# Performance work log

Hardware: AMD Instinct MI355X
Metric: run time of the kernel (lower is better)

The kernel has to match this reference:

```python
import jax, jax.numpy as jnp
import numpy as np


def conv2d(x, w, b=None):
    # NCHW conv, stride 1, 'same' padding inferred from kernel size
    ph, pw = w.shape[2] // 2, w.shape[3] // 2
    y = jax.lax.conv_general_dilated(
        x, w, window_strides=(1, 1), padding=[(ph, ph), (pw, pw)],
        dimension_numbers=('NCHW', 'OIHW', 'NCHW'))
    if b is not None:
        y = y + b[None, :, None, None]
    return y


def gelu(v):
    return jax.nn.gelu(v, approximate=False)  # torch nn.GELU default (erf)


def lrelu(v):
    return jnp.where(v >= 0, v, 0.1 * v)  # LeakyReLU(0.1)


def setup_inputs() -> dict:
    key = jax.random.key(0)
    ks = jax.random.split(key, 16)
    B, C, H, W = 2, 32, 256, 256
    s = 0.05
    return {
        'x':      jax.random.normal(ks[0], (B, C, H, W), jnp.float32),
        'key':    jax.random.normal(ks[1], (B, C, H, W), jnp.float32),
        'w_off1': jax.random.normal(ks[2], (32, 64, 3, 3), jnp.float32) * s,
        'b_off1': jax.random.normal(ks[3], (32,), jnp.float32) * s,
        'w_off2': jax.random.normal(ks[4], (32, 32, 3, 3), jnp.float32) * s,
        'b_off2': jax.random.normal(ks[5], (32,), jnp.float32) * s,
        'w_dcn':  jax.random.normal(ks[6], (288, 64, 3, 3), jnp.float32) * s,
        'b_dcn':  jax.random.normal(ks[7], (288,), jnp.float32) * s,
        'w_sel':  jax.random.normal(ks[8], (1, 3, 3, 3), jnp.float32) * s,
        'b_sel':  jax.random.normal(ks[9], (1,), jnp.float32) * s,
        'w_t1':   jax.random.normal(ks[10], (32, 32, 3, 3), jnp.float32) * s,
        'w_t2':   jax.random.normal(ks[11], (128, 32, 1, 1), jnp.float32) * s,
        'w_t3':   jax.random.normal(ks[12], (128, 128, 3, 3), jnp.float32) * s,
        'w_t4':   jax.random.normal(ks[13], (32, 128, 1, 1), jnp.float32) * s,
        'w_t5':   jax.random.normal(ks[14], (32, 32, 3, 3), jnp.float32) * s,
    }


def reference(x, key, w_off1, b_off1, w_off2, b_off2, w_dcn, b_dcn,
              w_sel, b_sel, w_t1, w_t2, w_t3, w_t4, w_t5):
    B, C, H, W = x.shape
    TOPK = 3
    # offset branch
    off = lrelu(conv2d(jnp.concatenate([x, key], axis=1), w_off1, b_off1))
    off = lrelu(conv2d(off, w_off2, b_off2))
    # dcn_attention proxy: conv over (key, offset) producing C*9 candidate warps
    warp = conv2d(jnp.concatenate([key, off], axis=1), w_dcn, b_dcn)
    warp = warp.reshape(B, C, 9, H, W)
    # correlation of each of 9 candidates with x, per pixel
    corr = jnp.einsum('bcohw,bchw->bohw', warp, x)            # [B,9,H,W]
    corr = corr.reshape(B, 9, H * W).transpose(0, 2, 1)       # [B,HW,9]
    _, idx = jax.lax.top_k(corr, TOPK)                        # [B,HW,3]
    # gather selected candidates per pixel per channel
    warp_p = warp.reshape(B, C, 9, H * W).transpose(0, 3, 2, 1)   # [B,HW,9,C]
    sel = jnp.take_along_axis(warp_p, idx[..., None], axis=2)     # [B,HW,3,C]
    key_warp = sel.reshape(B, H, W, TOPK, C).transpose(0, 4, 3, 1, 2)
    key_warp = key_warp.reshape(B * C, TOPK, H, W)
    key_warp = conv2d(key_warp, w_sel, b_sel).reshape(B, C, H, W)
    # tail: conv-GELU bottleneck stack
    y = conv2d(key_warp, w_t1)
    y = conv2d(gelu(y), w_t2)
    y = conv2d(gelu(y), w_t3)
    y = conv2d(gelu(y), w_t4)
    y = conv2d(gelu(y), w_t5)
    return y
```

## Files before the change

kernel.cpp:

```cpp
#include <hip/hip_runtime.h>
#include <math.h>

static constexpr int H = 256, W = 256, HW = H * W;

typedef __attribute__((ext_vector_type(8))) _Float16 half8v;
typedef __attribute__((ext_vector_type(4))) _Float16 half4v;
typedef __attribute__((ext_vector_type(4))) float  float4v;

__device__ __forceinline__ float gelu_f(float v) {
  return 0.5f * v * (1.0f + erff(v * 0.70710678118654752440f));
}
template<int ACT>
__device__ __forceinline__ float apply_act(float v) {
  if constexpr (ACT == 1) return v >= 0.f ? v : 0.1f * v;
  if constexpr (ACT == 2) return gelu_f(v);
  return v;
}

template<int C>
__global__ __launch_bounds__(256)
void pack_k(const float* __restrict__ in, _Float16* __restrict__ hi, _Float16* __restrict__ lo)
{
  const int p = blockIdx.x * 256 + threadIdx.x;
  const int b = blockIdx.y;
  const float* ip = in + (size_t)b * C * HW + p;
  __attribute__((aligned(16))) _Float16 hv[C], lv[C];
  #pragma unroll
  for (int c = 0; c < C; ++c) {
    float v = ip[(size_t)c * HW];
    _Float16 h = (_Float16)v;
    hv[c] = h;
    lv[c] = (_Float16)((v - (float)h) * 2048.0f);
  }
  size_t ob = ((size_t)b * HW + p) * C;
  #pragma unroll
  for (int j = 0; j < C / 8; ++j) {
    *(half8v*)&hi[ob + j * 8] = *(half8v*)&hv[j * 8];
    *(half8v*)&lo[ob + j * 8] = *(half8v*)&lv[j * 8];
  }
}

__global__ __launch_bounds__(256)
void prep_w_k(const float* __restrict__ w, _Float16* __restrict__ hi,
              _Float16* __restrict__ lo, int OC, int CIN)
{
  int tid = blockIdx.x * 256 + threadIdx.x;
  if (tid >= OC * CIN * 9) return;
  int ci = tid % CIN; int r = tid / CIN; int oc = r % OC; int tap = r / OC;
  float v = w[((size_t)oc * CIN + ci) * 9 + tap];
  _Float16 h = (_Float16)v;
  hi[tid] = h;
  lo[tid] = (_Float16)((v - (float)h) * 2048.0f);
}

template<int CIN, int OC, int OCB, int ACT, int OMODE, int SPLIT>
__global__ __launch_bounds__(256)
void conv3x3_mfma_k(const _Float16* __restrict__ iH0, const _Float16* __restrict__ iL0,
                    const _Float16* __restrict__ iH1, const _Float16* __restrict__ iL1, int cin0,
                    const _Float16* __restrict__ wHi, const _Float16* __restrict__ wLo,
                    const float* __restrict__ bias,
                    float* __restrict__ outF, _Float16* __restrict__ oH, _Float16* __restrict__ oL)
{
  constexpr int NOF  = OCB / 16;
  constexpr int REC  = (SPLIT == 3) ? 64 : 32;
  constexpr int nOcg = OC / OCB;
  __shared__ _Float16 sB[6 * 66 * REC];

  const int l  = threadIdx.x & 63;
  const int wv = threadIdx.x >> 6;

  const int bid = blockIdx.x;
  const int xcd = bid & 7, q = bid >> 3;
  const int ocg  = q % nOcg;
  const int tIdx = (q / nOcg) * 8 + xcd;
  const int b   = tIdx >> 8;
  const int x0  = ((tIdx >> 6) & 3) * 64;
  const int y0  = (tIdx & 63) * 4;
  const int oc0 = ocg * OCB;

  float4v accP[NOF][4];
  float4v accQ[(SPLIT == 3) ? NOF : 1][4];
  #pragma unroll
  for (int j = 0; j < NOF; ++j)
    #pragma unroll
    for (int f = 0; f < 4; ++f) {
      accP[j][f] = (float4v){0.f, 0.f, 0.f, 0.f};
      if constexpr (SPLIT == 3) accQ[j][f] = (float4v){0.f, 0.f, 0.f, 0.f};
    }

  const int k8  = (l >> 4) * 8;
  const int ocl = l & 15;
  const int sq  = l & 3;
  const int spx = l >> 2;

  #pragma unroll 1
  for (int cc = 0; cc < CIN; cc += 32) {
    const _Float16 *cbH, *cbL;
    if (cc < cin0) {
      size_t o = (size_t)(b * (cin0 >> 5) + (cc >> 5)) * HW * 32;
      cbH = iH0 + o; cbL = iL0 + o;
    } else {
      size_t o = (size_t)(b * ((CIN - cin0) >> 5) + ((cc - cin0) >> 5)) * HW * 32;
      cbH = iH1 + o; cbL = iL1 + o;
    }
    __syncthreads();
    if constexpr (SPLIT == 3) {
      #pragma unroll 2
      for (int t = wv; t < 60; t += 4) {
        int r = t / 10; int rem = t - r * 10; int bsel = rem / 5; int s = rem - bsel * 5;
        const _Float16* src = bsel ? cbL : cbH;
        int gy = y0 + r - 1;
        bool vy = (gy >= 0) && (gy < H);
        int gyc = gy < 0 ? 0 : (gy >= H ? H - 1 : gy);
        int pxl = s * 16 + spx;
        bool lact = (s < 4) || (l < 8);
        int gx = x0 + pxl - 1;
        bool vx = (gx >= 0) && (gx < W);
        int gxc = gx < 0 ? 0 : (gx >= W ? W - 1 : gx);
        half8v v;
        #pragma unroll
        for (int i = 0; i < 8; ++i) v[i] = (_Float16)0;
        if (lact && vy && vx)
          v = *(const half8v*)&src[((size_t)gyc * W + gxc) * 32 + sq * 8];
        int cls = (sq + (bsel ? 4 : 0)) ^ (pxl & 7);
        if (lact)
          *(half8v*)&sB[(r * 66 + pxl) * 64 + cls * 8] = v;
      }
    } else {
      #pragma unroll 2
      for (int t = wv; t < 30; t += 4) {
        int r = t / 5; int s = t - r * 5;
        int gy = y0 + r - 1;
        bool vy = (gy >= 0) && (gy < H);
        int gyc = gy < 0 ? 0 : (gy >= H ? H - 1 : gy);
        int pxl = s * 16 + spx;
        bool lact = (s < 4) || (l < 8);
        int gx = x0 + pxl - 1;
        bool vx = (gx >= 0) && (gx < W);
        int gxc = gx < 0 ? 0 : (gx >= W ? W - 1 : gx);
        half8v v;
        #pragma unroll
        for (int i = 0; i < 8; ++i) v[i] = (_Float16)0;
        if (lact && vy && vx)
          v = *(const half8v*)&cbH[((size_t)gyc * W + gxc) * 32 + sq * 8];
        int cls = (sq ^ pxl) & 3;
        if (lact)
          *(half8v*)&sB[(r * 66 + pxl) * 32 + cls * 8] = v;
      }
    }
    __syncthreads();

    #pragma unroll 1
    for (int tap = 0; tap < 9; ++tap) {
      const int dy = tap / 3, dx = tap - 3 * (tap / 3);
      half8v ah[NOF], aq[(SPLIT == 3) ? NOF : 1];
      const _Float16* hp = wHi + ((size_t)tap * OC + oc0 + ocl) * CIN + cc + k8;
      #pragma unroll
      for (int j = 0; j < NOF; ++j)
        ah[j] = *(const half8v*)(hp + (size_t)j * 16 * CIN);
      if constexpr (SPLIT == 3) {
        const _Float16* lp = wLo + ((size_t)tap * OC + oc0 + ocl) * CIN + cc + k8;
        #pragma unroll
        for (int j = 0; j < NOF; ++j)
          aq[j] = *(const half8v*)(lp + (size_t)j * 16 * CIN);
      }
      const int px = ocl + dx;
      if constexpr (SPLIT == 3) {
        const int rbase = ((wv + dy) * 66 + px) * 64;
        const int clsH = (l >> 4) ^ (px & 7);
        const int clsQ = ((l >> 4) + 4) ^ (px & 7);
        #pragma unroll
        for (int f = 0; f < 4; ++f) {
          half8v bh = *(const half8v*)&sB[rbase + f * 1024 + clsH * 8];
          half8v bq = *(const half8v*)&sB[rbase + f * 1024 + clsQ * 8];
          #pragma unroll
          for (int j = 0; j < NOF; ++j) {
            accP[j][f] = __builtin_amdgcn_mfma_f32_16x16x32_f16(ah[j], bh, accP[j][f], 0, 0, 0);
            accQ[j][f] = __builtin_amdgcn_mfma_f32_16x16x32_f16(ah[j], bq, accQ[j][f], 0, 0, 0);
            accQ[j][f] = __builtin_amdgcn_mfma_f32_16x16x32_f16(aq[j], bh, accQ[j][f], 0, 0, 0);
          }
        }
      } else {
        const int rbase = ((wv + dy) * 66 + px) * 32;
        const int clsH = ((l >> 4) ^ px) & 3;
        #pragma unroll
        for (int f = 0; f < 4; ++f) {
          half8v bh = *(const half8v*)&sB[rbase + f * 512 + clsH * 8];
          #pragma unroll
          for (int j = 0; j < NOF; ++j)
            accP[j][f] = __builtin_amdgcn_mfma_f32_16x16x32_f16(ah[j], bh, accP[j][f], 0, 0, 0);
        }
      }
    }
  }

  #pragma unroll
  for (int j = 0; j < NOF; ++j)
    #pragma unroll
    for (int f = 0; f < 4; ++f) {
      const int px  = x0 + f * 16 + ocl;
      const int occ = oc0 + j * 16 + (l >> 4) * 4;
      float vv4[4];
      #pragma unroll
      for (int r = 0; r < 4; ++r) {
        float bv = bias ? bias[occ + r] : 0.f;
        float vv = accP[j][f][r] + bv;
        if constexpr (SPLIT == 3) vv += accQ[j][f][r] * (1.0f / 2048.0f);
        vv4[r] = apply_act<ACT>(vv);
      }
      if constexpr (OMODE == 0) {
        #pragma unroll
        for (int r = 0; r < 4; ++r)
          outF[((size_t)(b * OC + occ + r) * H + (y0 + wv)) * W + px] = vv4[r];
      } else if constexpr (OMODE == 1) {
        __attribute__((aligned(8))) _Float16 hv[4], lv[4];
        #pragma unroll
        for (int r = 0; r < 4; ++r) {
          _Float16 h = (_Float16)vv4[r];
          hv[r] = h;
          lv[r] = (_Float16)((vv4[r] - (float)h) * 2048.0f);
        }
        size_t ob = ((size_t)b * HW + (size_t)(y0 + wv) * W + px) * OC + occ;
        *(half4v*)&oH[ob] = *(half4v*)&hv[0];
        *(half4v*)&oL[ob] = *(half4v*)&lv[0];
      } else {
        float4 v4;
        v4.x = vv4[0]; v4.y = vv4[1]; v4.z = vv4[2]; v4.w = vv4[3];
        *(float4*)&outF[((size_t)b * HW + (size_t)(y0 + wv) * W + px) * OC + occ] = v4;
      }
    }
}

template<int CIN, int OCB, int ACT, bool WLO>
__global__ __launch_bounds__(256)
void conv1x1_nhwc_k(const float* __restrict__ in, const float* __restrict__ w,
                    _Float16* __restrict__ oH, _Float16* __restrict__ oL, int OC)
{
  __shared__ __align__(16) float sW[OCB][CIN];
  const int b   = blockIdx.y;
  const int oc0 = blockIdx.z * OCB;
  for (int t = threadIdx.x; t < OCB * CIN; t += 256)
    sW[t / CIN][t % CIN] = w[(size_t)(oc0 + t / CIN) * CIN + (t % CIN)];
  __syncthreads();

  const int pb = blockIdx.x * 1024 + threadIdx.x;
  float acc[OCB][4];
  #pragma unroll
  for (int o = 0; o < OCB; ++o)
    #pragma unroll
    for (int i = 0; i < 4; ++i) acc[o][i] = 0.f;

  #pragma unroll 1
  for (int c0 = 0; c0 < CIN; c0 += 8) {
    float v[4][8];
    #pragma unroll
    for (int i = 0; i < 4; ++i) {
      const float* ip = in + ((size_t)b * HW + pb + i * 256) * CIN + c0;
      float4 a = *(const float4*)ip;
      float4 c = *(const float4*)(ip + 4);
      v[i][0]=a.x; v[i][1]=a.y; v[i][2]=a.z; v[i][3]=a.w;
      v[i][4]=c.x; v[i][5]=c.y; v[i][6]=c.z; v[i][7]=c.w;
    }
    #pragma unroll
    for (int o = 0; o < OCB; ++o) {
      const float4 w0 = *(const float4*)&sW[o][c0];
      const float4 w1 = *(const float4*)&sW[o][c0 + 4];
      #pragma unroll
      for (int i = 0; i < 4; ++i) {
        acc[o][i] += v[i][0]*w0.x + v[i][1]*w0.y + v[i][2]*w0.z + v[i][3]*w0.w
                   + v[i][4]*w1.x + v[i][5]*w1.y + v[i][6]*w1.z + v[i][7]*w1.w;
      }
    }
  }
  #pragma unroll
  for (int i = 0; i < 4; ++i) {
    __attribute__((aligned(16))) _Float16 hv[OCB], lv[OCB];
    #pragma unroll
    for (int o = 0; o < OCB; ++o) {
      float vv = apply_act<ACT>(acc[o][i]);
      _Float16 h = (_Float16)vv;
      hv[o] = h;
      if constexpr (WLO) lv[o] = (_Float16)((vv - (float)h) * 2048.0f);
    }
    size_t ob = ((size_t)(b * (OC >> 5) + (oc0 >> 5)) * HW + pb + i * 256) * 32 + (oc0 & 31);
    #pragma unroll
    for (int j = 0; j < OCB / 8; ++j) {
      *(half8v*)&oH[ob + j * 8] = *(half8v*)&hv[j * 8];
      if constexpr (WLO) *(half8v*)&oL[ob + j * 8] = *(half8v*)&lv[j * 8];
    }
  }
}

__global__ __launch_bounds__(256)
void corr_topk_k(const float* __restrict__ warp, const float* __restrict__ x,
                 int* __restrict__ idxo)
{
  const int p = blockIdx.x * 256 + threadIdx.x;
  const int b = blockIdx.y;
  float corr[9];
  #pragma unroll
  for (int o = 0; o < 9; ++o) corr[o] = 0.f;
  #pragma unroll 2
  for (int c = 0; c < 32; ++c) {
    float xv = x[((size_t)b * 32 + c) * HW + p];
    const float* wp = warp + ((size_t)b * 288 + (size_t)c * 9) * HW + p;
    #pragma unroll
    for (int o = 0; o < 9; ++o) corr[o] += wp[(size_t)o * HW] * xv;
  }
  unsigned mask = 0;
  int packed = 0;
  #pragma unroll
  for (int t = 0; t < 3; ++t) {
    float best = -INFINITY; int bi = 0;
    #pragma unroll
    for (int o = 0; o < 9; ++o) {
      bool take = (((mask >> o) & 1u) == 0u) && (corr[o] > best);
      best = take ? corr[o] : best;
      bi   = take ? o       : bi;
    }
    mask   |= 1u << bi;
    packed |= bi << (4 * t);
  }
  idxo[(size_t)b * HW + p] = packed;
}

__global__ __launch_bounds__(256)
void selconv_k(const float* __restrict__ warp, const int* __restrict__ idxp,
               const float* __restrict__ wsel, const float* __restrict__ bsel,
               _Float16* __restrict__ oH)
{
  const int tx = threadIdx.x & 31, ty = threadIdx.x >> 5;
  const int px = blockIdx.x * 32 + tx;
  const int py = blockIdx.y * 8 + ty;
  const int b  = blockIdx.z;

  int  nidx[9];
  bool nval[9];
  int  qoff[9];
  #pragma unroll
  for (int kh = 0; kh < 3; ++kh)
    #pragma unroll
    for (int kw = 0; kw < 3; ++kw) {
      int k = kh * 3 + kw;
      int qy = py + kh - 1, qx = px + kw - 1;
      nval[k] = (qy >= 0 && qy < H && qx >= 0 && qx < W);
      qoff[k] = qy * W + qx;
      nidx[k] = nval[k] ? idxp[(size_t)b * HW + qoff[k]] : 0;
    }

  float ws27[27];
  #pragma unroll
  for (int i = 0; i < 27; ++i) ws27[i] = wsel[i];
  const float bs = bsel[0];

  float arr[32];
  #pragma unroll 1
  for (int c = 0; c < 32; ++c) {
    float acc = bs;
    const float* wb = warp + ((size_t)b * 288 + (size_t)c * 9) * HW;
    #pragma unroll
    for (int k = 0; k < 9; ++k) {
      if (nval[k]) {
        int pk = nidx[k];
        #pragma unroll
        for (int t = 0; t < 3; ++t) {
          int o = (pk >> (4 * t)) & 15;
          acc += ws27[t * 9 + k] * wb[(size_t)o * HW + qoff[k]];
        }
      }
    }
    arr[c] = acc;
  }

  __attribute__((aligned(16))) _Float16 hv[32];
  #pragma unroll
  for (int c = 0; c < 32; ++c) hv[c] = (_Float16)arr[c];
  size_t ob = ((size_t)b * HW + (size_t)py * W + px) * 32;
  #pragma unroll
  for (int j = 0; j < 4; ++j)
    *(half8v*)&oH[ob + j * 8] = *(half8v*)&hv[j * 8];
}

extern "C" void kernel_launch(void* const* d_in, const int* in_sizes, int n_in,
                              void* d_out, int out_size, void* d_ws, size_t ws_size,
                              hipStream_t stream) {
  const float* x      = (const float*)d_in[0];
  const float* key    = (const float*)d_in[1];
  const float* w_off1 = (const float*)d_in[2];
  const float* b_off1 = (const float*)d_in[3];
  const float* w_off2 = (const float*)d_in[4];
  const float* b_off2 = (const float*)d_in[5];
  const float* w_dcn  = (const float*)d_in[6];
  const float* b_dcn  = (const float*)d_in[7];
  const float* w_sel  = (const float*)d_in[8];
  const float* b_sel  = (const float*)d_in[9];
  const float* w_t1   = (const float*)d_in[10];
  const float* w_t2   = (const float*)d_in[11];
  const float* w_t3   = (const float*)d_in[12];
  const float* w_t4   = (const float*)d_in[13];
  const float* w_t5   = (const float*)d_in[14];

  char* ws = (char*)d_ws;
  float* warp = (float*)(ws);
  _Float16* xH  = (_Float16*)(ws);
  _Float16* xL  = (_Float16*)(ws + 8388608);
  _Float16* o1H = (_Float16*)(ws + 16777216);
  _Float16* o1L = (_Float16*)(ws + 25165824);
  _Float16* w1H = (_Float16*)(ws + 33554432);
  _Float16* w1L = w1H + 18432;
  _Float16* w2H = w1L + 18432;
  _Float16* w2L = w2H + 9216;
  _Float16* kH  = (_Float16*)(ws + 150994944);
  _Float16* kL  = (_Float16*)(ws + 159383552);
  _Float16* o2H = (_Float16*)(ws + 167772160);
  _Float16* o2L = (_Float16*)(ws + 176160768);
  _Float16* wdH = (_Float16*)(ws + 184549376);
  _Float16* wdL = wdH + 165888;
  int*      idxb = (int*)(ws + 150994944);
  _Float16* kwH  = (_Float16*)(ws + 159383552);
  _Float16* twB  = (_Float16*)(ws + 176160768);
  _Float16* t1H_w = twB;
  _Float16* t1L_w = twB + 9216;
  _Float16* t3H_w = twB + 18432;
  _Float16* t3L_w = twB + 165888;
  _Float16* t5H_w = twB + 313344;
  _Float16* t5L_w = twB + 322560;
  float*    y1  = (float*)(ws);
  _Float16* t2H = (_Float16*)(ws + 16777216);
  float*    y3  = (float*)(ws + 83886080);
  _Float16* t4H = (_Float16*)(ws + 50331648);
  float* out = (float*)d_out;

  dim3 blk(256);

  pack_k<32><<<dim3(256, 2), blk, 0, stream>>>(x, xH, xL);
  pack_k<32><<<dim3(256, 2), blk, 0, stream>>>(key, kH, kL);
  prep_w_k<<<dim3(72),  blk, 0, stream>>>(w_off1, w1H, w1L, 32, 64);
  prep_w_k<<<dim3(36),  blk, 0, stream>>>(w_off2, w2H, w2L, 32, 32);
  prep_w_k<<<dim3(648), blk, 0, stream>>>(w_dcn,  wdH, wdL, 288, 64);

  conv3x3_mfma_k<64, 32, 32, 1, 1, 3><<<dim3(512), blk, 0, stream>>>(
      xH, xL, kH, kL, 32, w1H, w1L, b_off1, nullptr, o1H, o1L);
  conv3x3_mfma_k<32, 32, 32, 1, 1, 3><<<dim3(512), blk, 0, stream>>>(
      o1H, o1L, o1H, o1L, 32, w2H, w2L, b_off2, nullptr, o2H, o2L);
  conv3x3_mfma_k<64, 288, 48, 0, 0, 3><<<dim3(3072), blk, 0, stream>>>(
      kH, kL, o2H, o2L, 32, wdH, wdL, b_dcn, warp, nullptr, nullptr);
  corr_topk_k<<<dim3(256, 2), blk, 0, stream>>>(warp, x, idxb);
  selconv_k<<<dim3(8, 32, 2), blk, 0, stream>>>(warp, idxb, w_sel, b_sel, kwH);

  prep_w_k<<<dim3(36),  blk, 0, stream>>>(w_t1, t1H_w, t1L_w, 32, 32);
  prep_w_k<<<dim3(576), blk, 0, stream>>>(w_t3, t3H_w, t3L_w, 128, 128);
  prep_w_k<<<dim3(36),  blk, 0, stream>>>(w_t5, t5H_w, t5L_w, 32, 32);

  conv3x3_mfma_k<32, 32, 32, 2, 2, 1><<<dim3(512), blk, 0, stream>>>(
      kwH, kwH, kwH, kwH, 32, t1H_w, t1L_w, nullptr, y1, nullptr, nullptr);
  conv1x1_nhwc_k<32, 16, 2, false><<<dim3(64, 2, 8), blk, 0, stream>>>(y1, w_t2, t2H, nullptr, 128);
  conv3x3_mfma_k<128, 128, 64, 2, 2, 1><<<dim3(1024), blk, 0, stream>>>(
      t2H, t2H, t2H, t2H, 128, t3H_w, t3L_w, nullptr, y3, nullptr, nullptr);
  conv1x1_nhwc_k<128, 16, 2, false><<<dim3(64, 2, 2), blk, 0, stream>>>(y3, w_t4, t4H, nullptr, 32);
  conv3x3_mfma_k<32, 32, 32, 0, 0, 1><<<dim3(512), blk, 0, stream>>>(
      t4H, t4H, t4H, t4H, 32, t5H_w, t5L_w, nullptr, out, nullptr, nullptr);
}
```

Before: 717.8 us.

## Load conv input tiles directly from global memory, drop LDS staging, merge prep kernels

```diff
diff --git a/kernel.cpp b/kernel.cpp
--- a/kernel.cpp
+++ b/kernel.cpp
@@ -6,6 +6,13 @@
 typedef __attribute__((ext_vector_type(8))) _Float16 half8v;
 typedef __attribute__((ext_vector_type(4))) _Float16 half4v;
 typedef __attribute__((ext_vector_type(4))) float  float4v;
+
+__device__ __forceinline__ half8v h8zero() {
+  half8v z;
+  #pragma unroll
+  for (int i = 0; i < 8; ++i) z[i] = (_Float16)0;
+  return z;
+}
 
 __device__ __forceinline__ float gelu_f(float v) {
   return 0.5f * v * (1.0f + erff(v * 0.70710678118654752440f));
@@ -17,34 +24,35 @@
   return v;
 }
 
-template<int C>
-__global__ __launch_bounds__(256)
-void pack_k(const float* __restrict__ in, _Float16* __restrict__ hi, _Float16* __restrict__ lo)
+__global__ __launch_bounds__(256)
+void pack2_k(const float* __restrict__ inA, _Float16* __restrict__ hiA, _Float16* __restrict__ loA,
+             const float* __restrict__ inB, _Float16* __restrict__ hiB, _Float16* __restrict__ loB)
 {
   const int p = blockIdx.x * 256 + threadIdx.x;
   const int b = blockIdx.y;
-  const float* ip = in + (size_t)b * C * HW + p;
-  __attribute__((aligned(16))) _Float16 hv[C], lv[C];
-  #pragma unroll
-  for (int c = 0; c < C; ++c) {
+  const float* in = blockIdx.z ? inB : inA;
+  _Float16* hi = blockIdx.z ? hiB : hiA;
+  _Float16* lo = blockIdx.z ? loB : loA;
+  const float* ip = in + (size_t)b * 32 * HW + p;
+  __attribute__((aligned(16))) _Float16 hv[32], lv[32];
+  #pragma unroll
+  for (int c = 0; c < 32; ++c) {
     float v = ip[(size_t)c * HW];
     _Float16 h = (_Float16)v;
     hv[c] = h;
     lv[c] = (_Float16)((v - (float)h) * 2048.0f);
   }
-  size_t ob = ((size_t)b * HW + p) * C;
-  #pragma unroll
-  for (int j = 0; j < C / 8; ++j) {
+  size_t ob = ((size_t)b * HW + p) * 32;
+  #pragma unroll
+  for (int j = 0; j < 4; ++j) {
     *(half8v*)&hi[ob + j * 8] = *(half8v*)&hv[j * 8];
     *(half8v*)&lo[ob + j * 8] = *(half8v*)&lv[j * 8];
   }
 }
 
-__global__ __launch_bounds__(256)
-void prep_w_k(const float* __restrict__ w, _Float16* __restrict__ hi,
-              _Float16* __restrict__ lo, int OC, int CIN)
-{
-  int tid = blockIdx.x * 256 + threadIdx.x;
+__device__ __forceinline__ void prep_w_body(const float* w, _Float16* hi, _Float16* lo,
+                                            int OC, int CIN, int tid)
+{
   if (tid >= OC * CIN * 9) return;
   int ci = tid % CIN; int r = tid / CIN; int oc = r % OC; int tap = r / OC;
   float v = w[((size_t)oc * CIN + ci) * 9 + tap];
@@ -52,6 +60,16 @@
   hi[tid] = h;
   lo[tid] = (_Float16)((v - (float)h) * 2048.0f);
 }
+__global__ __launch_bounds__(256)
+void prep3_w_k(const float* __restrict__ w0, _Float16* __restrict__ h0, _Float16* __restrict__ l0, int OC0, int CIN0, int nb0,
+               const float* __restrict__ w1, _Float16* __restrict__ h1, _Float16* __restrict__ l1, int OC1, int CIN1, int nb1,
+               const float* __restrict__ w2, _Float16* __restrict__ h2, _Float16* __restrict__ l2, int OC2, int CIN2)
+{
+  int bb = blockIdx.x;
+  if (bb < nb0)            prep_w_body(w0, h0, l0, OC0, CIN0, bb * 256 + threadIdx.x);
+  else if (bb < nb0 + nb1) prep_w_body(w1, h1, l1, OC1, CIN1, (bb - nb0) * 256 + threadIdx.x);
+  else                     prep_w_body(w2, h2, l2, OC2, CIN2, (bb - nb0 - nb1) * 256 + threadIdx.x);
+}
 
 template<int CIN, int OC, int OCB, int ACT, int OMODE, int SPLIT>
 __global__ __launch_bounds__(256)
@@ -62,9 +80,7 @@
                     float* __restrict__ outF, _Float16* __restrict__ oH, _Float16* __restrict__ oL)
 {
   constexpr int NOF  = OCB / 16;
-  constexpr int REC  = (SPLIT == 3) ? 64 : 32;
   constexpr int nOcg = OC / OCB;
-  __shared__ _Float16 sB[6 * 66 * REC];
 
   const int l  = threadIdx.x & 63;
   const int wv = threadIdx.x >> 6;
@@ -90,8 +106,7 @@
 
   const int k8  = (l >> 4) * 8;
   const int ocl = l & 15;
-  const int sq  = l & 3;
-  const int spx = l >> 2;
+  const int rowy = y0 + wv;
 
   #pragma unroll 1
   for (int cc = 0; cc < CIN; cc += 32) {
@@ -103,56 +118,29 @@
       size_t o = (size_t)(b * ((CIN - cin0) >> 5) + ((cc - cin0) >> 5)) * HW * 32;
       cbH = iH1 + o; cbL = iL1 + o;
     }
-    __syncthreads();
-    if constexpr (SPLIT == 3) {
-      #pragma unroll 2
-      for (int t = wv; t < 60; t += 4) {
-        int r = t / 10; int rem = t - r * 10; int bsel = rem / 5; int s = rem - bsel * 5;
-        const _Float16* src = bsel ? cbL : cbH;
-        int gy = y0 + r - 1;
-        bool vy = (gy >= 0) && (gy < H);
-        int gyc = gy < 0 ? 0 : (gy >= H ? H - 1 : gy);
-        int pxl = s * 16 + spx;
-        bool lact = (s < 4) || (l < 8);
-        int gx = x0 + pxl - 1;
-        bool vx = (gx >= 0) && (gx < W);
-        int gxc = gx < 0 ? 0 : (gx >= W ? W - 1 : gx);
-        half8v v;
-        #pragma unroll
-        for (int i = 0; i < 8; ++i) v[i] = (_Float16)0;
-        if (lact && vy && vx)
-          v = *(const half8v*)&src[((size_t)gyc * W + gxc) * 32 + sq * 8];
-        int cls = (sq + (bsel ? 4 : 0)) ^ (pxl & 7);
-        if (lact)
-          *(half8v*)&sB[(r * 66 + pxl) * 64 + cls * 8] = v;
-      }
-    } else {
-      #pragma unroll 2
-      for (int t = wv; t < 30; t += 4) {
-        int r = t / 5; int s = t - r * 5;
-        int gy = y0 + r - 1;
-        bool vy = (gy >= 0) && (gy < H);
-        int gyc = gy < 0 ? 0 : (gy >= H ? H - 1 : gy);
-        int pxl = s * 16 + spx;
-        bool lact = (s < 4) || (l < 8);
-        int gx = x0 + pxl - 1;
-        bool vx = (gx >= 0) && (gx < W);
-        int gxc = gx < 0 ? 0 : (gx >= W ? W - 1 : gx);
-        half8v v;
-        #pragma unroll
-        for (int i = 0; i < 8; ++i) v[i] = (_Float16)0;
-        if (lact && vy && vx)
-          v = *(const half8v*)&cbH[((size_t)gyc * W + gxc) * 32 + sq * 8];
-        int cls = (sq ^ pxl) & 3;
-        if (lact)
-          *(half8v*)&sB[(r * 66 + pxl) * 32 + cls * 8] = v;
-      }
-    }
-    __syncthreads();
 
     #pragma unroll 1
     for (int tap = 0; tap < 9; ++tap) {
-      const int dy = tap / 3, dx = tap - 3 * (tap / 3);
+      const int dy = tap / 3, dx = tap - 3 * dy;
+      const int gy = rowy + dy - 1;
+      const bool vy = (gy >= 0) && (gy < H);
+      const int gyc = gy < 0 ? 0 : (gy >= H ? H - 1 : gy);
+      const size_t rowb = (size_t)gyc * W;
+
+      half8v bh[4], bq[(SPLIT == 3) ? 4 : 1];
+      #pragma unroll
+      for (int f = 0; f < 4; ++f) {
+        int gx = x0 + f * 16 + ocl + dx - 1;
+        bool ok = vy && ((unsigned)gx < (unsigned)W);
+        int gxc = gx < 0 ? 0 : (gx >= W ? W - 1 : gx);
+        size_t a = (rowb + gxc) * 32 + k8;
+        half8v vh = *(const half8v*)&cbH[a];
+        bh[f] = ok ? vh : h8zero();
+        if constexpr (SPLIT == 3) {
+          half8v vl = *(const half8v*)&cbL[a];
+          bq[f] = ok ? vl : h8zero();
+        }
+      }
       half8v ah[NOF], aq[(SPLIT == 3) ? NOF : 1];
       const _Float16* hp = wHi + ((size_t)tap * OC + oc0 + ocl) * CIN + cc + k8;
       #pragma unroll
@@ -164,31 +152,15 @@
         for (int j = 0; j < NOF; ++j)
           aq[j] = *(const half8v*)(lp + (size_t)j * 16 * CIN);
       }
-      const int px = ocl + dx;
-      if constexpr (SPLIT == 3) {
-        const int rbase = ((wv + dy) * 66 + px) * 64;
-        const int clsH = (l >> 4) ^ (px & 7);
-        const int clsQ = ((l >> 4) + 4) ^ (px & 7);
+      #pragma unroll
+      for (int f = 0; f < 4; ++f) {
         #pragma unroll
-        for (int f = 0; f < 4; ++f) {
-          half8v bh = *(const half8v*)&sB[rbase + f * 1024 + clsH * 8];
-          half8v bq = *(const half8v*)&sB[rbase + f * 1024 + clsQ * 8];
-          #pragma unroll
-          for (int j = 0; j < NOF; ++j) {
-            accP[j][f] = __builtin_amdgcn_mfma_f32_16x16x32_f16(ah[j], bh, accP[j][f], 0, 0, 0);
-            accQ[j][f] = __builtin_amdgcn_mfma_f32_16x16x32_f16(ah[j], bq, accQ[j][f], 0, 0, 0);
-            accQ[j][f] = __builtin_amdgcn_mfma_f32_16x16x32_f16(aq[j], bh, accQ[j][f], 0, 0, 0);
+        for (int j = 0; j < NOF; ++j) {
+          accP[j][f] = __builtin_amdgcn_mfma_f32_16x16x32_f16(ah[j], bh[f], accP[j][f], 0, 0, 0);
+          if constexpr (SPLIT == 3) {
+            accQ[j][f] = __builtin_amdgcn_mfma_f32_16x16x32_f16(ah[j], bq[f], accQ[j][f], 0, 0, 0);
+            accQ[j][f] = __builtin_amdgcn_mfma_f32_16x16x32_f16(aq[j], bh[f], accQ[j][f], 0, 0, 0);
           }
-        }
-      } else {
-        const int rbase = ((wv + dy) * 66 + px) * 32;
-        const int clsH = ((l >> 4) ^ px) & 3;
-        #pragma unroll
-        for (int f = 0; f < 4; ++f) {
-          half8v bh = *(const half8v*)&sB[rbase + f * 512 + clsH * 8];
-          #pragma unroll
-          for (int j = 0; j < NOF; ++j)
-            accP[j][f] = __builtin_amdgcn_mfma_f32_16x16x32_f16(ah[j], bh, accP[j][f], 0, 0, 0);
         }
       }
     }
@@ -211,7 +183,7 @@
       if constexpr (OMODE == 0) {
         #pragma unroll
         for (int r = 0; r < 4; ++r)
-          outF[((size_t)(b * OC + occ + r) * H + (y0 + wv)) * W + px] = vv4[r];
+          outF[((size_t)(b * OC + occ + r) * H + rowy) * W + px] = vv4[r];
       } else if constexpr (OMODE == 1) {
         __attribute__((aligned(8))) _Float16 hv[4], lv[4];
         #pragma unroll
@@ -220,21 +192,21 @@
           hv[r] = h;
           lv[r] = (_Float16)((vv4[r] - (float)h) * 2048.0f);
         }
-        size_t ob = ((size_t)b * HW + (size_t)(y0 + wv) * W + px) * OC + occ;
+        size_t ob = ((size_t)b * HW + (size_t)rowy * W + px) * OC + occ;
         *(half4v*)&oH[ob] = *(half4v*)&hv[0];
         *(half4v*)&oL[ob] = *(half4v*)&lv[0];
       } else {
         float4 v4;
         v4.x = vv4[0]; v4.y = vv4[1]; v4.z = vv4[2]; v4.w = vv4[3];
-        *(float4*)&outF[((size_t)b * HW + (size_t)(y0 + wv) * W + px) * OC + occ] = v4;
-      }
-    }
-}
-
-template<int CIN, int OCB, int ACT, bool WLO>
+        *(float4*)&outF[((size_t)b * HW + (size_t)rowy * W + px) * OC + occ] = v4;
+      }
+    }
+}
+
+template<int CIN, int OCB, int ACT>
 __global__ __launch_bounds__(256)
 void conv1x1_nhwc_k(const float* __restrict__ in, const float* __restrict__ w,
-                    _Float16* __restrict__ oH, _Float16* __restrict__ oL, int OC)
+                    _Float16* __restrict__ oH, int OC)
 {
   __shared__ __align__(16) float sW[OCB][CIN];
   const int b   = blockIdx.y;
@@ -274,20 +246,14 @@
   }
   #pragma unroll
   for (int i = 0; i < 4; ++i) {
-    __attribute__((aligned(16))) _Float16 hv[OCB], lv[OCB];
-    #pragma unroll
-    for (int o = 0; o < OCB; ++o) {
-      float vv = apply_act<ACT>(acc[o][i]);
-      _Float16 h = (_Float16)vv;
-      hv[o] = h;
-      if constexpr (WLO) lv[o] = (_Float16)((vv - (float)h) * 2048.0f);
-    }
+    __attribute__((aligned(16))) _Float16 hv[OCB];
+    #pragma unroll
+    for (int o = 0; o < OCB; ++o)
+      hv[o] = (_Float16)apply_act<ACT>(acc[o][i]);
     size_t ob = ((size_t)(b * (OC >> 5) + (oc0 >> 5)) * HW + pb + i * 256) * 32 + (oc0 & 31);
     #pragma unroll
-    for (int j = 0; j < OCB / 8; ++j) {
+    for (int j = 0; j < OCB / 8; ++j)
       *(half8v*)&oH[ob + j * 8] = *(half8v*)&hv[j * 8];
-      if constexpr (WLO) *(half8v*)&oL[ob + j * 8] = *(half8v*)&lv[j * 8];
-    }
   }
 }
 
@@ -433,31 +399,32 @@
 
   dim3 blk(256);
 
-  pack_k<32><<<dim3(256, 2), blk, 0, stream>>>(x, xH, xL);
-  pack_k<32><<<dim3(256, 2), blk, 0, stream>>>(key, kH, kL);
-  prep_w_k<<<dim3(72),  blk, 0, stream>>>(w_off1, w1H, w1L, 32, 64);
-  prep_w_k<<<dim3(36),  blk, 0, stream>>>(w_off2, w2H, w2L, 32, 32);
-  prep_w_k<<<dim3(648), blk, 0, stream>>>(w_dcn,  wdH, wdL, 288, 64);
+  pack2_k<<<dim3(256, 2, 2), blk, 0, stream>>>(x, xH, xL, key, kH, kL);
+  prep3_w_k<<<dim3(756), blk, 0, stream>>>(
+      w_off1, w1H, w1L, 32, 64, 72,
+      w_off2, w2H, w2L, 32, 32, 36,
+      w_dcn,  wdH, wdL, 288, 64);
 
   conv3x3_mfma_k<64, 32, 32, 1, 1, 3><<<dim3(512), blk, 0, stream>>>(
       xH, xL, kH, kL, 32, w1H, w1L, b_off1, nullptr, o1H, o1L);
   conv3x3_mfma_k<32, 32, 32, 1, 1, 3><<<dim3(512), blk, 0, stream>>>(
       o1H, o1L, o1H, o1L, 32, w2H, w2L, b_off2, nullptr, o2H, o2L);
-  conv3x3_mfma_k<64, 288, 48, 0, 0, 3><<<dim3(3072), blk, 0, stream>>>(
+  conv3x3_mfma_k<64, 288, 32, 0, 0, 3><<<dim3(4608), blk, 0, stream>>>(
       kH, kL, o2H, o2L, 32, wdH, wdL, b_dcn, warp, nullptr, nullptr);
   corr_topk_k<<<dim3(256, 2), blk, 0, stream>>>(warp, x, idxb);
   selconv_k<<<dim3(8, 32, 2), blk, 0, stream>>>(warp, idxb, w_sel, b_sel, kwH);
 
-  prep_w_k<<<dim3(36),  blk, 0, stream>>>(w_t1, t1H_w, t1L_w, 32, 32);
-  prep_w_k<<<dim3(576), blk, 0, stream>>>(w_t3, t3H_w, t3L_w, 128, 128);
-  prep_w_k<<<dim3(36),  blk, 0, stream>>>(w_t5, t5H_w, t5L_w, 32, 32);
+  prep3_w_k<<<dim3(648), blk, 0, stream>>>(
+      w_t1, t1H_w, t1L_w, 32, 32, 36,
+      w_t3, t3H_w, t3L_w, 128, 128, 576,
+      w_t5, t5H_w, t5L_w, 32, 32);
 
   conv3x3_mfma_k<32, 32, 32, 2, 2, 1><<<dim3(512), blk, 0, stream>>>(
       kwH, kwH, kwH, kwH, 32, t1H_w, t1L_w, nullptr, y1, nullptr, nullptr);
-  conv1x1_nhwc_k<32, 16, 2, false><<<dim3(64, 2, 8), blk, 0, stream>>>(y1, w_t2, t2H, nullptr, 128);
+  conv1x1_nhwc_k<32, 16, 2><<<dim3(64, 2, 8), blk, 0, stream>>>(y1, w_t2, t2H, 128);
   conv3x3_mfma_k<128, 128, 64, 2, 2, 1><<<dim3(1024), blk, 0, stream>>>(
       t2H, t2H, t2H, t2H, 128, t3H_w, t3L_w, nullptr, y3, nullptr, nullptr);
-  conv1x1_nhwc_k<128, 16, 2, false><<<dim3(64, 2, 2), blk, 0, stream>>>(y3, w_t4, t4H, nullptr, 32);
+  conv1x1_nhwc_k<128, 16, 2><<<dim3(64, 2, 2), blk, 0, stream>>>(y3, w_t4, t4H, 32);
   conv3x3_mfma_k<32, 32, 32, 0, 0, 1><<<dim3(512), blk, 0, stream>>>(
       t4H, t4H, t4H, t4H, 32, t5H_w, t5L_w, nullptr, out, nullptr, nullptr);
 }
```

New measurement: 793.3 us. 1.11x slower.
